# Kernel tuning notes

Measured on AMD Instinct MI355X. Metric: run time of the kernel, lower is better.

The kernel has to match this reference:

```python
import jax, jax.numpy as jnp
import numpy as np

QLEN, MLEN = 1024, 1024
KLEN = QLEN + MLEN
BSZ = 2
D_MODEL = 1024
N_HEAD, D_HEAD = 16, 64


def setup_inputs() -> dict:
    key = jax.random.key(0)
    ks = jax.random.split(key, 8)
    s = 0.02
    return {
        "w": jax.random.normal(ks[0], (KLEN, BSZ, D_MODEL), jnp.float32),
        "r": jax.random.normal(ks[1], (KLEN, D_MODEL), jnp.float32),
        "r_w_bias": jax.random.normal(ks[2], (N_HEAD, D_HEAD), jnp.float32) * s,
        "r_r_bias": jax.random.normal(ks[3], (N_HEAD, D_HEAD), jnp.float32) * s,
        "Wq": jax.random.normal(ks[4], (D_MODEL, N_HEAD * D_HEAD), jnp.float32) * s,
        "Wkv": jax.random.normal(ks[5], (D_MODEL, 2 * N_HEAD * D_HEAD), jnp.float32) * s,
        "Wr": jax.random.normal(ks[6], (D_MODEL, N_HEAD * D_HEAD), jnp.float32) * s,
        "Wo": jax.random.normal(ks[7], (N_HEAD * D_HEAD, D_MODEL), jnp.float32) * s,
        "qlen": QLEN,
    }


def _rel_shift(x):
    # x: [qlen, klen, bsz, n_head]. Pad one zero column at the front of the
    # key axis, reinterpret flat layout as [klen+1, qlen, ...], drop row 0.
    q, k, b, n = x.shape
    x_pad = jnp.pad(x, ((0, 0), (1, 0), (0, 0), (0, 0)))
    return x_pad.reshape(k + 1, q, b, n)[1:].reshape(q, k, b, n)


def reference(w, r, r_w_bias, r_r_bias, Wq, Wkv, Wr, Wo, qlen):
    klen, bsz, _ = w.shape
    rlen = r.shape[0]
    scale = 1.0 / (D_HEAD ** 0.5)

    w_head_q = (w[-qlen:] @ Wq).reshape(qlen, bsz, N_HEAD, D_HEAD)
    kv = w @ Wkv
    w_head_k = kv[..., : N_HEAD * D_HEAD].reshape(klen, bsz, N_HEAD, D_HEAD)
    w_head_v = kv[..., N_HEAD * D_HEAD :].reshape(klen, bsz, N_HEAD, D_HEAD)
    r_head_k = (r @ Wr).reshape(rlen, N_HEAD, D_HEAD)

    AC = jnp.einsum("ibnd,jbnd->ijbn", w_head_q + r_w_bias, w_head_k)
    BD = jnp.einsum("ibnd,jnd->ijbn", w_head_q + r_r_bias, r_head_k)
    attn_score = (AC + _rel_shift(BD)) * scale

    attn_prob = jax.nn.softmax(attn_score, axis=1)
    attn_vec = jnp.einsum("ijbn,jbnd->ibnd", attn_prob, w_head_v)
    attn_vec = attn_vec.reshape(qlen, bsz, N_HEAD * D_HEAD)
    return attn_vec @ Wo
```

## Files before the change

### kernel.cpp

```cpp
#include <hip/hip_runtime.h>
#include <hip/hip_bf16.h>


#define QLENC 1024
#define KLENC 2048
#define BSZC 2
#define DMODELC 1024
#define NHC 16
#define DHC 64

typedef _Float16 half_t;
typedef __attribute__((ext_vector_type(8))) _Float16 f16x8;
typedef __attribute__((ext_vector_type(4))) float f32x4;

__device__ __forceinline__ void async_copy16(const half_t* g, half_t* l) {
    __builtin_amdgcn_global_load_lds(
        (const __attribute__((address_space(1))) void*)g,
        (__attribute__((address_space(3))) void*)l,
        16, 0, 0);
}

__global__ __launch_bounds__(256) void prep(
    const float* __restrict__ w, const float* __restrict__ r,
    const float* __restrict__ Wq, const float* __restrict__ Wkv,
    const float* __restrict__ Wr, const float* __restrict__ Wo,
    half_t* __restrict__ wh, half_t* __restrict__ rh,
    half_t* __restrict__ WqT, half_t* __restrict__ WkvT,
    half_t* __restrict__ WrT, half_t* __restrict__ WoT) {
    __shared__ __attribute__((aligned(16))) half_t T[64][72];
    int bx = blockIdx.x, t = threadIdx.x;
    if (bx < 3072) {
        const float* s; half_t* d; size_t base;
        if (bx < 2048) { s = w; d = wh; base = (size_t)bx * 2048; }
        else           { s = r; d = rh; base = (size_t)(bx - 2048) * 2048; }
        size_t i = base + (size_t)t * 8;
        const float4* sp = (const float4*)(s + i);
        float4 f0 = sp[0], f1 = sp[1];
        half_t h[8];
        h[0] = (half_t)f0.x; h[1] = (half_t)f0.y; h[2] = (half_t)f0.z; h[3] = (half_t)f0.w;
        h[4] = (half_t)f1.x; h[5] = (half_t)f1.y; h[6] = (half_t)f1.z; h[7] = (half_t)f1.w;
        *(uint4*)(d + i) = *(uint4*)&h[0];
        return;
    }
    int b2 = bx - 3072;
    const float* W; half_t* Wt; int N, tx, ty;
    if (b2 < 256)       { W = Wq;  Wt = WqT;  N = 1024; tx = b2 & 15;         ty = b2 >> 4; }
    else if (b2 < 768)  { int c = b2 - 256;  W = Wkv; Wt = WkvT; N = 2048; tx = c & 31; ty = c >> 5; }
    else if (b2 < 1024) { int c = b2 - 768;  W = Wr;  Wt = WrT;  N = 1024; tx = c & 15; ty = c >> 4; }
    else                { int c = b2 - 1024; W = Wo;  Wt = WoT;  N = 1024; tx = c & 15; ty = c >> 4; }
    const int K = 1024;
    int n0 = tx * 64, k0 = ty * 64;
    int r_ = t >> 2, c_ = (t & 3) << 4;
    const float4* s = (const float4*)&W[(size_t)(k0 + r_) * N + n0 + c_];
    float4 f0 = s[0], f1 = s[1], f2 = s[2], f3 = s[3];
    half_t h[16];
    h[0] = (half_t)f0.x; h[1] = (half_t)f0.y; h[2] = (half_t)f0.z; h[3] = (half_t)f0.w;
    h[4] = (half_t)f1.x; h[5] = (half_t)f1.y; h[6] = (half_t)f1.z; h[7] = (half_t)f1.w;
    h[8] = (half_t)f2.x; h[9] = (half_t)f2.y; h[10] = (half_t)f2.z; h[11] = (half_t)f2.w;
    h[12] = (half_t)f3.x; h[13] = (half_t)f3.y; h[14] = (half_t)f3.z; h[15] = (half_t)f3.w;
    *(uint4*)&T[r_][c_] = *(uint4*)&h[0];
    *(uint4*)&T[r_][c_ + 8] = *(uint4*)&h[8];
    __syncthreads();
    half_t vals[16];
#pragma unroll
    for (int u = 0; u < 16; u++) vals[u] = T[c_ + u][r_];
    *(uint4*)&Wt[(size_t)(n0 + r_) * K + k0 + c_] = *(uint4*)&vals[0];
    *(uint4*)&Wt[(size_t)(n0 + r_) * K + k0 + c_ + 8] = *(uint4*)&vals[8];
}

__global__ __launch_bounds__(256) void proj_fused(
    const half_t* __restrict__ wh, const half_t* __restrict__ rh,
    const half_t* __restrict__ WqT, const half_t* __restrict__ WkvT,
    const half_t* __restrict__ WrT,
    half_t* __restrict__ qw, half_t* __restrict__ qr,
    half_t* __restrict__ kh, half_t* __restrict__ vt,
    half_t* __restrict__ rk,
    const float* __restrict__ rwb, const float* __restrict__ rrb) {
    __shared__ __attribute__((aligned(16))) half_t SM[128 * 136];
    half_t (*As)[64] = (half_t(*)[64])SM;
    half_t (*Bs)[64] = (half_t(*)[64])(SM + 128 * 64);
    half_t (*LT)[136] = (half_t(*)[136])SM;

    int bid = blockIdx.x;
    int mode, tx, ty;
    const half_t* A; const half_t* Bt;
    if (bid < 512)      { mode = 1; tx = bid & 15, ty = bid >> 4; A = wh; Bt = WkvT; }
    else if (bid < 640) { int c = bid - 512; mode = 0; tx = c & 7; ty = c >> 3;
                          A = wh + (size_t)QLENC * BSZC * DMODELC; Bt = WqT; }
    else                { int c = bid - 640; mode = 2; tx = c & 7; ty = c >> 3;
                          A = rh; Bt = WrT; }

    int t = threadIdx.x;
    int w = t >> 6, ln = t & 63, quad = ln >> 4, l15 = ln & 15;
    int m0 = ty * 128, n0 = tx * 128;
    int rbase = 64 * (w >> 1), cbase = 64 * (w & 1);
    int lrow = ln >> 3, lcol = (ln & 7) * 8;

    f32x4 acc[4][4];
#pragma unroll
    for (int i = 0; i < 4; i++)
#pragma unroll
        for (int j = 0; j < 4; j++) acc[i][j] = (f32x4){0.f, 0.f, 0.f, 0.f};

    for (int k0 = 0; k0 < 1024; k0 += 64) {
        __syncthreads();
#pragma unroll
        for (int j = 0; j < 4; j++) {
            int r8 = w * 32 + j * 8;
            async_copy16(&A[(size_t)(m0 + r8 + lrow) * 1024 + k0 + lcol], &As[r8][0]);
            async_copy16(&Bt[(size_t)(n0 + r8 + lrow) * 1024 + k0 + lcol], &Bs[r8][0]);
        }
        __syncthreads();
#pragma unroll
        for (int kk = 0; kk < 2; kk++) {
            f16x8 af[4], bfr[4];
#pragma unroll
            for (int rb = 0; rb < 4; rb++)
                af[rb] = *(const f16x8*)&As[rbase + rb * 16 + l15][kk * 32 + quad * 8];
#pragma unroll
            for (int cb = 0; cb < 4; cb++)
                bfr[cb] = *(const f16x8*)&Bs[cbase + cb * 16 + l15][kk * 32 + quad * 8];
#pragma unroll
            for (int rb = 0; rb < 4; rb++)
#pragma unroll
                for (int cb = 0; cb < 4; cb++)
                    acc[rb][cb] = __builtin_amdgcn_mfma_f32_16x16x32_f16(
                        af[rb], bfr[cb], acc[rb][cb], 0, 0, 0);
        }
    }

    if (mode == 1 && tx >= 8) {
        __syncthreads();
#pragma unroll
        for (int rb = 0; rb < 4; rb++)
#pragma unroll
            for (int cb = 0; cb < 4; cb++)
#pragma unroll
                for (int reg = 0; reg < 4; reg++) {
                    int lr_ = rbase + 16 * rb + quad * 4 + reg;
                    int lc_ = cbase + 16 * cb + l15;
                    LT[lc_][lr_] = (half_t)acc[rb][cb][reg];
                }
        __syncthreads();
#pragma unroll
        for (int pass = 0; pass < 8; pass++) {
            int g = pass * 32 + (t >> 3), s_ = t & 7;
            int lc_ = g >> 1, b_ = g & 1;
            half_t tmp[8];
#pragma unroll
            for (int k = 0; k < 8; k++) tmp[k] = LT[lc_][b_ + 2 * (s_ * 8 + k)];
            int gc = n0 - 1024 + lc_;
            int hh = gc >> 6, d_ = gc & 63;
            int p0 = (m0 >> 1) + s_ * 8;
            *(uint4*)&vt[(((size_t)(b_ * NHC + hh)) * DHC + d_) * KLENC + p0] = *(uint4*)&tmp[0];
        }
        return;
    }

#pragma unroll
    for (int rb = 0; rb < 4; rb++)
#pragma unroll
        for (int cb = 0; cb < 4; cb++)
#pragma unroll
            for (int reg = 0; reg < 4; reg++) {
                int gr = m0 + rbase + 16 * rb + quad * 4 + reg;
                int gc = n0 + cbase + 16 * cb + l15;
                float v = acc[rb][cb][reg];
                if (mode == 1) {
                    int p_ = gr >> 1, b_ = gr & 1;
                    int n_ = gc >> 6, d_ = gc & 63;
                    kh[(((size_t)(b_ * NHC + n_)) * KLENC + p_) * DHC + d_] = (half_t)v;
                } else if (mode == 0) {
                    int p_ = gr >> 1, b_ = gr & 1, n_ = gc >> 6, d_ = gc & 63;
                    size_t idx = (((size_t)(b_ * NHC + n_)) * QLENC + p_) * DHC + d_;
                    qw[idx] = (half_t)(v + rwb[gc]);
                    qr[idx] = (half_t)(v + rrb[gc]);
                } else {
                    int n_ = gc >> 6, d_ = gc & 63;
                    rk[(((size_t)n_) * KLENC + gr) * DHC + d_] = (half_t)v;
                }
            }
}

__global__ __launch_bounds__(256) void gemm_out(
    const half_t* __restrict__ A, const half_t* __restrict__ Bt,
    float* __restrict__ o) {
    __shared__ __attribute__((aligned(16))) half_t As[128][64];
    __shared__ __attribute__((aligned(16))) half_t Bs[128][64];

    int t = threadIdx.x;
    int w = t >> 6, ln = t & 63, quad = ln >> 4, l15 = ln & 15;
    int m0 = blockIdx.y * 128, n0 = blockIdx.x * 128;
    int rbase = 64 * (w >> 1), cbase = 64 * (w & 1);
    int lrow = ln >> 3, lcol = (ln & 7) * 8;

    f32x4 acc[4][4];
#pragma unroll
    for (int i = 0; i < 4; i++)
#pragma unroll
        for (int j = 0; j < 4; j++) acc[i][j] = (f32x4){0.f, 0.f, 0.f, 0.f};

    for (int k0 = 0; k0 < 1024; k0 += 64) {
        __syncthreads();
#pragma unroll
        for (int j = 0; j < 4; j++) {
            int r8 = w * 32 + j * 8;
            async_copy16(&A[(size_t)(m0 + r8 + lrow) * 1024 + k0 + lcol], &As[r8][0]);
            async_copy16(&Bt[(size_t)(n0 + r8 + lrow) * 1024 + k0 + lcol], &Bs[r8][0]);
        }
        __syncthreads();
#pragma unroll
        for (int kk = 0; kk < 2; kk++) {
            f16x8 af[4], bfr[4];
#pragma unroll
            for (int rb = 0; rb < 4; rb++)
                af[rb] = *(const f16x8*)&As[rbase + rb * 16 + l15][kk * 32 + quad * 8];
#pragma unroll
            for (int cb = 0; cb < 4; cb++)
                bfr[cb] = *(const f16x8*)&Bs[cbase + cb * 16 + l15][kk * 32 + quad * 8];
#pragma unroll
            for (int rb = 0; rb < 4; rb++)
#pragma unroll
                for (int cb = 0; cb < 4; cb++)
                    acc[rb][cb] = __builtin_amdgcn_mfma_f32_16x16x32_f16(
                        af[rb], bfr[cb], acc[rb][cb], 0, 0, 0);
        }
    }

#pragma unroll
    for (int rb = 0; rb < 4; rb++)
#pragma unroll
        for (int cb = 0; cb < 4; cb++)
#pragma unroll
            for (int reg = 0; reg < 4; reg++) {
                int gr = m0 + rbase + 16 * rb + quad * 4 + reg;
                int gc = n0 + cbase + 16 * cb + l15;
                o[(size_t)gr * 1024 + gc] = acc[rb][cb][reg];
            }
}

__global__ __launch_bounds__(256, 3) void attn_fused(
    const half_t* __restrict__ qw, const half_t* __restrict__ qr,
    const half_t* __restrict__ kh, const half_t* __restrict__ vt,
    const half_t* __restrict__ rk, half_t* __restrict__ av) {
    __shared__ __attribute__((aligned(16))) half_t Ks[64][72];
    __shared__ __attribute__((aligned(16))) half_t Vs[64][72];
    __shared__ __attribute__((aligned(16))) half_t RKs[128][72];
    __shared__ __attribute__((aligned(16))) half_t TP[4][16][88];

    int n = blockIdx.x, i0 = blockIdx.y * 64, b = blockIdx.z;
    int t = threadIdx.x, w = t >> 6, ln = t & 63, quad = ln >> 4, l15 = ln & 15;
    int lr = t >> 2, lc = (t & 3) << 4;
    int q4 = quad * 4;
    int wq = w * 16 + q4;
    size_t bn = (size_t)(b * NHC + n);
    const half_t* rkn = rk + (size_t)n * KLENC * DHC;
    half_t (*TPw)[88] = TP[w];

    f16x8 aqw[2], aq1[2], aq2[2];
    {
        int row1 = i0 + w * 16 + l15;
        int row2 = row1 + 1; if (row2 > QLENC - 1) row2 = QLENC - 1;
#pragma unroll
        for (int kk = 0; kk < 2; kk++) {
            aqw[kk] = *(const f16x8*)&qw[((bn * QLENC) + row1) * DHC + kk * 32 + quad * 8];
            aq1[kk] = *(const f16x8*)&qr[((bn * QLENC) + row1) * DHC + kk * 32 + quad * 8];
            aq2[kk] = *(const f16x8*)&qr[((bn * QLENC) + row2) * DHC + kk * 32 + quad * 8];
        }
    }

    int rrl = t >> 1, rh = (t & 1) * 32;

    uint4 pk0, pk1, pv0, pv1, pr0, pr1, pr2, pr3;
    {
        int D = 0 - i0;
        int mb = (D <= 1024) ? (960 + D) : (D - 1089);
        int rrow = mb + rrl; rrow = rrow < 0 ? 0 : (rrow > KLENC - 1 ? KLENC - 1 : rrow);
        const uint4* ks = (const uint4*)&kh[((bn * KLENC) + 0 + lr) * DHC + lc];
        const uint4* vs = (const uint4*)&vt[((bn * DHC) + lr) * KLENC + 0 + lc];
        pk0 = ks[0]; pk1 = ks[1]; pv0 = vs[0]; pv1 = vs[1];
        const uint4* rs = (const uint4*)&rkn[(size_t)rrow * DHC + rh];
        pr0 = rs[0]; pr1 = rs[1]; pr2 = rs[2]; pr3 = rs[3];
    }

    f32x4 O[4];
#pragma unroll
    for (int i = 0; i < 4; i++) O[i] = (f32x4){0.f, 0.f, 0.f, 0.f};
    float lsum[4] = {0.f, 0.f, 0.f, 0.f};
    const float scale = 0.125f;

    for (int jt = 0; jt < KLENC / 64; jt++) {
        int j0 = jt * 64;
        int D = j0 - i0;
        bool need1 = (D <= 1024), need2 = (D >= 1024);

        __syncthreads();
        *(uint4*)&Ks[lr][lc] = pk0; *(uint4*)&Ks[lr][lc + 8] = pk1;
        *(uint4*)&Vs[lr][lc] = pv0; *(uint4*)&Vs[lr][lc + 8] = pv1;
        *(uint4*)&RKs[rrl][rh] = pr0;      *(uint4*)&RKs[rrl][rh + 8] = pr1;
        *(uint4*)&RKs[rrl][rh + 16] = pr2; *(uint4*)&RKs[rrl][rh + 24] = pr3;
        __syncthreads();

        if (jt + 1 < KLENC / 64) {
            int j0n = j0 + 64, Dn = j0n - i0;
            int mbn = (Dn <= 1024) ? (960 + Dn) : (Dn - 1089);
            int rrown = mbn + rrl; rrown = rrown < 0 ? 0 : (rrown > KLENC - 1 ? KLENC - 1 : rrown);
            const uint4* ks = (const uint4*)&kh[((bn * KLENC) + j0n + lr) * DHC + lc];
            const uint4* vs = (const uint4*)&vt[((bn * DHC) + lr) * KLENC + j0n + lc];
            pk0 = ks[0]; pk1 = ks[1]; pv0 = vs[0]; pv1 = vs[1];
            const uint4* rs = (const uint4*)&rkn[(size_t)rrown * DHC + rh];
            pr0 = rs[0]; pr1 = rs[1]; pr2 = rs[2]; pr3 = rs[3];
        }

        f32x4 sa[4];
#pragma unroll
        for (int cb = 0; cb < 4; cb++) sa[cb] = (f32x4){0.f, 0.f, 0.f, 0.f};
#pragma unroll
        for (int kk = 0; kk < 2; kk++) {
#pragma unroll
            for (int cb = 0; cb < 4; cb++) {
                f16x8 bk = *(const f16x8*)&Ks[cb * 16 + l15][kk * 32 + quad * 8];
                sa[cb] = __builtin_amdgcn_mfma_f32_16x16x32_f16(aqw[kk], bk, sa[cb], 0, 0, 0);
            }
        }

        float bdv[4][4];
#pragma unroll
        for (int cb = 0; cb < 4; cb++)
#pragma unroll
            for (int reg = 0; reg < 4; reg++) bdv[cb][reg] = 0.f;

        if (need1) {
            f32x4 tacc[5];
#pragma unroll
            for (int c = 0; c < 5; c++) tacc[c] = (f32x4){0.f, 0.f, 0.f, 0.f};
#pragma unroll
            for (int kk = 0; kk < 2; kk++) {
#pragma unroll
                for (int c = 0; c < 5; c++) {
                    f16x8 bk = *(const f16x8*)&RKs[(3 - w + c) * 16 + l15][kk * 32 + quad * 8];
                    tacc[c] = __builtin_amdgcn_mfma_f32_16x16x32_f16(aq1[kk], bk, tacc[c], 0, 0, 0);
                }
            }
#pragma unroll
            for (int c = 0; c < 5; c++)
#pragma unroll
                for (int reg = 0; reg < 4; reg++)
                    TPw[q4 + reg][c * 16 + l15] = (half_t)tacc[c][reg];
#pragma unroll
            for (int reg = 0; reg < 4; reg++) {
                int icl = q4 + reg, ic = w * 16 + icl;
#pragma unroll
                for (int cb = 0; cb < 4; cb++) {
                    int jc = cb * 16 + l15;
                    int delta = D + jc - ic;
                    if (delta <= 1024) bdv[cb][reg] = (float)TPw[icl][15 + jc - icl];
                }
            }
        }
        if (need2) {
            if (need1) {
                int mb2 = D - 1089;
                int rrow2 = mb2 + rrl; rrow2 = rrow2 < 0 ? 0 : (rrow2 > KLENC - 1 ? KLENC - 1 : rrow2);
                const uint4* rs2 = (const uint4*)&rkn[(size_t)rrow2 * DHC + rh];
                uint4 t0 = rs2[0], t1 = rs2[1], t2 = rs2[2], t3 = rs2[3];
                __syncthreads();
                *(uint4*)&RKs[rrl][rh] = t0;      *(uint4*)&RKs[rrl][rh + 8] = t1;
                *(uint4*)&RKs[rrl][rh + 16] = t2; *(uint4*)&RKs[rrl][rh + 24] = t3;
                __syncthreads();
            }
            f32x4 tacc[5];
#pragma unroll
            for (int c = 0; c < 5; c++) tacc[c] = (f32x4){0.f, 0.f, 0.f, 0.f};
#pragma unroll
            for (int kk = 0; kk < 2; kk++) {
#pragma unroll
                for (int c = 0; c < 5; c++) {
                    f16x8 bk = *(const f16x8*)&RKs[(3 - w + c) * 16 + l15][kk * 32 + quad * 8];
                    tacc[c] = __builtin_amdgcn_mfma_f32_16x16x32_f16(aq2[kk], bk, tacc[c], 0, 0, 0);
                }
            }
#pragma unroll
            for (int c = 0; c < 5; c++)
#pragma unroll
                for (int reg = 0; reg < 4; reg++)
                    TPw[q4 + reg][c * 16 + l15] = (half_t)tacc[c][reg];
#pragma unroll
            for (int reg = 0; reg < 4; reg++) {
                int icl = q4 + reg, ic = w * 16 + icl;
#pragma unroll
                for (int cb = 0; cb < 4; cb++) {
                    int jc = cb * 16 + l15;
                    int delta = D + jc - ic;
                    if (delta >= 1026) bdv[cb][reg] = (float)TPw[icl][15 + jc - icl];
                }
            }
        }

        float p[4][4];
#pragma unroll
        for (int reg = 0; reg < 4; reg++) {
            float ps = 0.f;
#pragma unroll
            for (int cb = 0; cb < 4; cb++) {
                float e = __expf((sa[cb][reg] + bdv[cb][reg]) * scale);
                e = fminf(e, 60000.f);
                p[cb][reg] = e; ps += e;
            }
            lsum[reg] += ps;
        }

#pragma unroll
        for (int cb = 0; cb < 4; cb++)
#pragma unroll
            for (int reg = 0; reg < 4; reg++)
                TPw[q4 + reg][cb * 16 + l15] = (half_t)p[cb][reg];
#pragma unroll
        for (int kk = 0; kk < 2; kk++) {
            f16x8 pa = *(const f16x8*)&TPw[l15][kk * 32 + quad * 8];
#pragma unroll
            for (int db = 0; db < 4; db++) {
                f16x8 vb = *(const f16x8*)&Vs[db * 16 + l15][kk * 32 + quad * 8];
                O[db] = __builtin_amdgcn_mfma_f32_16x16x32_f16(pa, vb, O[db], 0, 0, 0);
            }
        }
    }

    float inv[4];
#pragma unroll
    for (int reg = 0; reg < 4; reg++) {
        float tot = lsum[reg];
#pragma unroll
        for (int off = 1; off < 16; off <<= 1) tot += __shfl_xor(tot, off, 64);
        inv[reg] = 1.0f / tot;
    }
#pragma unroll
    for (int db = 0; db < 4; db++)
#pragma unroll
        for (int reg = 0; reg < 4; reg++) {
            int i = i0 + wq + reg;
            int col = n * 64 + db * 16 + l15;
            av[((size_t)i * BSZC + b) * DMODELC + col] = (half_t)(O[db][reg] * inv[reg]);
        }
}

extern "C" void kernel_launch(void* const* d_in, const int* in_sizes, int n_in,
                              void* d_out, int out_size, void* d_ws, size_t ws_size,
                              hipStream_t stream) {
    const float* w   = (const float*)d_in[0];
    const float* r   = (const float*)d_in[1];
    const float* rwb = (const float*)d_in[2];
    const float* rrb = (const float*)d_in[3];
    const float* Wq  = (const float*)d_in[4];
    const float* Wkv = (const float*)d_in[5];
    const float* Wr  = (const float*)d_in[6];
    const float* Wo  = (const float*)d_in[7];
    float* out = (float*)d_out;

    half_t* ws = (half_t*)d_ws;
    half_t* qw   = ws; ws += (size_t)BSZC * NHC * QLENC * DHC;
    half_t* qr   = ws; ws += (size_t)BSZC * NHC * QLENC * DHC;
    half_t* kh   = ws; ws += (size_t)BSZC * NHC * KLENC * DHC;
    half_t* vt   = ws; ws += (size_t)BSZC * NHC * KLENC * DHC;
    half_t* rk   = ws; ws += (size_t)NHC * KLENC * DHC;
    half_t* av   = ws; ws += (size_t)QLENC * BSZC * DMODELC;
    half_t* WqT  = ws; ws += (size_t)DMODELC * DMODELC;
    half_t* WkvT = ws; ws += (size_t)2 * DMODELC * DMODELC;
    half_t* WrT  = ws; ws += (size_t)DMODELC * DMODELC;
    half_t* WoT  = ws; ws += (size_t)DMODELC * DMODELC;
    half_t* wh   = ws; ws += (size_t)KLENC * BSZC * DMODELC;
    half_t* rh   = ws; ws += (size_t)KLENC * DMODELC;

    dim3 blk(256);
    prep<<<dim3(4352), blk, 0, stream>>>(w, r, Wq, Wkv, Wr, Wo,
                                         wh, rh, WqT, WkvT, WrT, WoT);
    proj_fused<<<dim3(768), blk, 0, stream>>>(
        wh, rh, WqT, WkvT, WrT, qw, qr, kh, vt, rk, rwb, rrb);
    attn_fused<<<dim3(NHC, QLENC / 64, BSZC), blk, 0, stream>>>(
        qw, qr, kh, vt, rk, av);
    gemm_out<<<dim3(8, 16), blk, 0, stream>>>(av, WoT, out);

    (void)in_sizes; (void)n_in; (void)out_size; (void)ws_size;
}
```

Baseline: 270.6 us.

## Double-buffer K/V in LDS and load relative keys directly into registers

```diff
diff --git a/kernel.cpp b/kernel.cpp
--- a/kernel.cpp
+++ b/kernel.cpp
@@ -239,13 +239,12 @@
             }
 }
 
-__global__ __launch_bounds__(256, 3) void attn_fused(
+__global__ __launch_bounds__(256, 2) void attn_fused(
     const half_t* __restrict__ qw, const half_t* __restrict__ qr,
     const half_t* __restrict__ kh, const half_t* __restrict__ vt,
     const half_t* __restrict__ rk, half_t* __restrict__ av) {
-    __shared__ __attribute__((aligned(16))) half_t Ks[64][72];
-    __shared__ __attribute__((aligned(16))) half_t Vs[64][72];
-    __shared__ __attribute__((aligned(16))) half_t RKs[128][72];
+    __shared__ __attribute__((aligned(16))) half_t Ks[2][64][72];
+    __shared__ __attribute__((aligned(16))) half_t Vs[2][64][72];
     __shared__ __attribute__((aligned(16))) half_t TP[4][16][88];
 
     int n = blockIdx.x, i0 = blockIdx.y * 64, b = blockIdx.z;
@@ -269,18 +268,26 @@
         }
     }
 
-    int rrl = t >> 1, rh = (t & 1) * 32;
-
-    uint4 pk0, pk1, pv0, pv1, pr0, pr1, pr2, pr3;
+#define LOAD_RK(MB, DST)                                                      \
+    do {                                                                      \
+        _Pragma("unroll")                                                     \
+        for (int c_ = 0; c_ < 5; c_++) {                                      \
+            int rg = (MB) + (3 - w + c_) * 16 + l15;                          \
+            rg = rg < 0 ? 0 : (rg > KLENC - 1 ? KLENC - 1 : rg);              \
+            const half_t* rp = &rkn[(size_t)rg * DHC + quad * 8];             \
+            DST[c_ * 2]     = *(const f16x8*)rp;                              \
+            DST[c_ * 2 + 1] = *(const f16x8*)(rp + 32);                       \
+        }                                                                     \
+    } while (0)
+
+    uint4 pk0, pk1, pv0, pv1;
+    f16x8 rka[10], rkb[10];
     {
-        int D = 0 - i0;
-        int mb = (D <= 1024) ? (960 + D) : (D - 1089);
-        int rrow = mb + rrl; rrow = rrow < 0 ? 0 : (rrow > KLENC - 1 ? KLENC - 1 : rrow);
         const uint4* ks = (const uint4*)&kh[((bn * KLENC) + 0 + lr) * DHC + lc];
         const uint4* vs = (const uint4*)&vt[((bn * DHC) + lr) * KLENC + 0 + lc];
         pk0 = ks[0]; pk1 = ks[1]; pv0 = vs[0]; pv1 = vs[1];
-        const uint4* rs = (const uint4*)&rkn[(size_t)rrow * DHC + rh];
-        pr0 = rs[0]; pr1 = rs[1]; pr2 = rs[2]; pr3 = rs[3];
+        int D0 = 0 - i0;
+        LOAD_RK(960 + D0, rka);
     }
 
     f32x4 O[4];
@@ -289,142 +296,128 @@
     float lsum[4] = {0.f, 0.f, 0.f, 0.f};
     const float scale = 0.125f;
 
-    for (int jt = 0; jt < KLENC / 64; jt++) {
-        int j0 = jt * 64;
-        int D = j0 - i0;
-        bool need1 = (D <= 1024), need2 = (D >= 1024);
-
-        __syncthreads();
-        *(uint4*)&Ks[lr][lc] = pk0; *(uint4*)&Ks[lr][lc + 8] = pk1;
-        *(uint4*)&Vs[lr][lc] = pv0; *(uint4*)&Vs[lr][lc + 8] = pv1;
-        *(uint4*)&RKs[rrl][rh] = pr0;      *(uint4*)&RKs[rrl][rh + 8] = pr1;
-        *(uint4*)&RKs[rrl][rh + 16] = pr2; *(uint4*)&RKs[rrl][rh + 24] = pr3;
-        __syncthreads();
-
-        if (jt + 1 < KLENC / 64) {
-            int j0n = j0 + 64, Dn = j0n - i0;
-            int mbn = (Dn <= 1024) ? (960 + Dn) : (Dn - 1089);
-            int rrown = mbn + rrl; rrown = rrown < 0 ? 0 : (rrown > KLENC - 1 ? KLENC - 1 : rrown);
-            const uint4* ks = (const uint4*)&kh[((bn * KLENC) + j0n + lr) * DHC + lc];
-            const uint4* vs = (const uint4*)&vt[((bn * DHC) + lr) * KLENC + j0n + lc];
-            pk0 = ks[0]; pk1 = ks[1]; pv0 = vs[0]; pv1 = vs[1];
-            const uint4* rs = (const uint4*)&rkn[(size_t)rrown * DHC + rh];
-            pr0 = rs[0]; pr1 = rs[1]; pr2 = rs[2]; pr3 = rs[3];
-        }
-
-        f32x4 sa[4];
-#pragma unroll
-        for (int cb = 0; cb < 4; cb++) sa[cb] = (f32x4){0.f, 0.f, 0.f, 0.f};
-#pragma unroll
-        for (int kk = 0; kk < 2; kk++) {
-#pragma unroll
-            for (int cb = 0; cb < 4; cb++) {
-                f16x8 bk = *(const f16x8*)&Ks[cb * 16 + l15][kk * 32 + quad * 8];
-                sa[cb] = __builtin_amdgcn_mfma_f32_16x16x32_f16(aqw[kk], bk, sa[cb], 0, 0, 0);
-            }
-        }
-
-        float bdv[4][4];
-#pragma unroll
-        for (int cb = 0; cb < 4; cb++)
-#pragma unroll
-            for (int reg = 0; reg < 4; reg++) bdv[cb][reg] = 0.f;
-
-        if (need1) {
-            f32x4 tacc[5];
-#pragma unroll
-            for (int c = 0; c < 5; c++) tacc[c] = (f32x4){0.f, 0.f, 0.f, 0.f};
-#pragma unroll
-            for (int kk = 0; kk < 2; kk++) {
-#pragma unroll
-                for (int c = 0; c < 5; c++) {
-                    f16x8 bk = *(const f16x8*)&RKs[(3 - w + c) * 16 + l15][kk * 32 + quad * 8];
-                    tacc[c] = __builtin_amdgcn_mfma_f32_16x16x32_f16(aq1[kk], bk, tacc[c], 0, 0, 0);
-                }
-            }
-#pragma unroll
-            for (int c = 0; c < 5; c++)
-#pragma unroll
-                for (int reg = 0; reg < 4; reg++)
-                    TPw[q4 + reg][c * 16 + l15] = (half_t)tacc[c][reg];
-#pragma unroll
-            for (int reg = 0; reg < 4; reg++) {
-                int icl = q4 + reg, ic = w * 16 + icl;
-#pragma unroll
-                for (int cb = 0; cb < 4; cb++) {
-                    int jc = cb * 16 + l15;
-                    int delta = D + jc - ic;
-                    if (delta <= 1024) bdv[cb][reg] = (float)TPw[icl][15 + jc - icl];
-                }
-            }
-        }
-        if (need2) {
-            if (need1) {
-                int mb2 = D - 1089;
-                int rrow2 = mb2 + rrl; rrow2 = rrow2 < 0 ? 0 : (rrow2 > KLENC - 1 ? KLENC - 1 : rrow2);
-                const uint4* rs2 = (const uint4*)&rkn[(size_t)rrow2 * DHC + rh];
-                uint4 t0 = rs2[0], t1 = rs2[1], t2 = rs2[2], t3 = rs2[3];
-                __syncthreads();
-                *(uint4*)&RKs[rrl][rh] = t0;      *(uint4*)&RKs[rrl][rh + 8] = t1;
-                *(uint4*)&RKs[rrl][rh + 16] = t2; *(uint4*)&RKs[rrl][rh + 24] = t3;
-                __syncthreads();
-            }
-            f32x4 tacc[5];
-#pragma unroll
-            for (int c = 0; c < 5; c++) tacc[c] = (f32x4){0.f, 0.f, 0.f, 0.f};
-#pragma unroll
-            for (int kk = 0; kk < 2; kk++) {
-#pragma unroll
-                for (int c = 0; c < 5; c++) {
-                    f16x8 bk = *(const f16x8*)&RKs[(3 - w + c) * 16 + l15][kk * 32 + quad * 8];
-                    tacc[c] = __builtin_amdgcn_mfma_f32_16x16x32_f16(aq2[kk], bk, tacc[c], 0, 0, 0);
-                }
-            }
-#pragma unroll
-            for (int c = 0; c < 5; c++)
-#pragma unroll
-                for (int reg = 0; reg < 4; reg++)
-                    TPw[q4 + reg][c * 16 + l15] = (half_t)tacc[c][reg];
-#pragma unroll
-            for (int reg = 0; reg < 4; reg++) {
-                int icl = q4 + reg, ic = w * 16 + icl;
-#pragma unroll
-                for (int cb = 0; cb < 4; cb++) {
-                    int jc = cb * 16 + l15;
-                    int delta = D + jc - ic;
-                    if (delta >= 1026) bdv[cb][reg] = (float)TPw[icl][15 + jc - icl];
-                }
-            }
-        }
-
-        float p[4][4];
-#pragma unroll
-        for (int reg = 0; reg < 4; reg++) {
-            float ps = 0.f;
-#pragma unroll
-            for (int cb = 0; cb < 4; cb++) {
-                float e = __expf((sa[cb][reg] + bdv[cb][reg]) * scale);
-                e = fminf(e, 60000.f);
-                p[cb][reg] = e; ps += e;
-            }
-            lsum[reg] += ps;
-        }
-
-#pragma unroll
-        for (int cb = 0; cb < 4; cb++)
-#pragma unroll
-            for (int reg = 0; reg < 4; reg++)
-                TPw[q4 + reg][cb * 16 + l15] = (half_t)p[cb][reg];
-#pragma unroll
-        for (int kk = 0; kk < 2; kk++) {
-            f16x8 pa = *(const f16x8*)&TPw[l15][kk * 32 + quad * 8];
-#pragma unroll
-            for (int db = 0; db < 4; db++) {
-                f16x8 vb = *(const f16x8*)&Vs[db * 16 + l15][kk * 32 + quad * 8];
-                O[db] = __builtin_amdgcn_mfma_f32_16x16x32_f16(pa, vb, O[db], 0, 0, 0);
-            }
-        }
-    }
+#define TILE_BODY(JT, BUF, RKC, RKN)                                          \
+    do {                                                                      \
+        int j0 = (JT) * 64;                                                   \
+        int D = j0 - i0;                                                      \
+        bool need1 = (D <= 1024), need2 = (D >= 1024);     \
+        *(uint4*)&Ks[BUF][lr][lc] = pk0; *(uint4*)&Ks[BUF][lr][lc + 8] = pk1; \
+        *(uint4*)&Vs[BUF][lr][lc] = pv0; *(uint4*)&Vs[BUF][lr][lc + 8] = pv1; \
+        __syncthreads();                                                      \
+        if ((JT) + 1 < KLENC / 64) {                                          \
+            int j0n = j0 + 64, Dn = j0n - i0;                                 \
+            const uint4* ksp = (const uint4*)&kh[((bn * KLENC) + j0n + lr) * DHC + lc]; \
+            const uint4* vsp = (const uint4*)&vt[((bn * DHC) + lr) * KLENC + j0n + lc]; \
+            pk0 = ksp[0]; pk1 = ksp[1]; pv0 = vsp[0]; pv1 = vsp[1];           \
+            int mbn = (Dn <= 1024) ? (960 + Dn) : (Dn - 1089);                \
+            LOAD_RK(mbn, RKN);                                                \
+        }                                                                     \
+        f32x4 sa[4];                                                          \
+        _Pragma("unroll")                                                     \
+        for (int cb = 0; cb < 4; cb++) sa[cb] = (f32x4){0.f, 0.f, 0.f, 0.f};  \
+        _Pragma("unroll")                                                     \
+        for (int kk = 0; kk < 2; kk++) {                                      \
+            _Pragma("unroll")                                                 \
+            for (int cb = 0; cb < 4; cb++) {                                  \
+                f16x8 bk = *(const f16x8*)&Ks[BUF][cb * 16 + l15][kk * 32 + quad * 8]; \
+                sa[cb] = __builtin_amdgcn_mfma_f32_16x16x32_f16(aqw[kk], bk, sa[cb], 0, 0, 0); \
+            }                                                                 \
+        }                                                                     \
+        float bdv[4][4];                                                      \
+        _Pragma("unroll")                                                     \
+        for (int cb = 0; cb < 4; cb++)                                        \
+            _Pragma("unroll")                                                 \
+            for (int reg = 0; reg < 4; reg++) bdv[cb][reg] = 0.f;             \
+        {    \
+            f16x8 aqA0 = need1 ? aq1[0] : aq2[0];                             \
+            f16x8 aqA1 = need1 ? aq1[1] : aq2[1];                             \
+            f32x4 tacc[5];                                                    \
+            _Pragma("unroll")                                                 \
+            for (int c = 0; c < 5; c++) tacc[c] = (f32x4){0.f, 0.f, 0.f, 0.f}; \
+            _Pragma("unroll")                                                 \
+            for (int c = 0; c < 5; c++) {                                     \
+                tacc[c] = __builtin_amdgcn_mfma_f32_16x16x32_f16(aqA0, RKC[c * 2], tacc[c], 0, 0, 0); \
+                tacc[c] = __builtin_amdgcn_mfma_f32_16x16x32_f16(aqA1, RKC[c * 2 + 1], tacc[c], 0, 0, 0); \
+            }                                                                 \
+            _Pragma("unroll")                                                 \
+            for (int c = 0; c < 5; c++)                                       \
+                _Pragma("unroll")                                             \
+                for (int reg = 0; reg < 4; reg++)                             \
+                    TPw[q4 + reg][c * 16 + l15] = (half_t)tacc[c][reg];       \
+            _Pragma("unroll")                                                 \
+            for (int reg = 0; reg < 4; reg++) {                               \
+                int icl = q4 + reg, ic = w * 16 + icl;                        \
+                _Pragma("unroll")                                             \
+                for (int cb = 0; cb < 4; cb++) {                              \
+                    int jc = cb * 16 + l15;                                   \
+                    int delta = D + jc - ic;                                  \
+                    bool take = need1 ? (delta <= 1024) : (delta >= 1026);    \
+                    if (take) bdv[cb][reg] = (float)TPw[icl][15 + jc - icl];  \
+                }                                                             \
+            }                                                                 \
+        }                                                                     \
+        if (need1 && need2) {     \
+            f16x8 rkm[10];                                                    \
+            LOAD_RK(D - 1089, rkm);                                           \
+            f32x4 tacc[5];                                                    \
+            _Pragma("unroll")                                                 \
+            for (int c = 0; c < 5; c++) tacc[c] = (f32x4){0.f, 0.f, 0.f, 0.f}; \
+            _Pragma("unroll")                                                 \
+            for (int c = 0; c < 5; c++) {                                     \
+                tacc[c] = __builtin_amdgcn_mfma_f32_16x16x32_f16(aq2[0], rkm[c * 2], tacc[c], 0, 0, 0); \
+                tacc[c] = __builtin_amdgcn_mfma_f32_16x16x32_f16(aq2[1], rkm[c * 2 + 1], tacc[c], 0, 0, 0); \
+            }                                                                 \
+            _Pragma("unroll")                                                 \
+            for (int c = 0; c < 5; c++)                                       \
+                _Pragma("unroll")                                             \
+                for (int reg = 0; reg < 4; reg++)                             \
+                    TPw[q4 + reg][c * 16 + l15] = (half_t)tacc[c][reg];       \
+            _Pragma("unroll")                                                 \
+            for (int reg = 0; reg < 4; reg++) {                               \
+                int icl = q4 + reg, ic = w * 16 + icl;                        \
+                _Pragma("unroll")                                             \
+                for (int cb = 0; cb < 4; cb++) {                              \
+                    int jc = cb * 16 + l15;                                   \
+                    int delta = D + jc - ic;                                  \
+                    if (delta >= 1026) bdv[cb][reg] = (float)TPw[icl][15 + jc - icl]; \
+                }                                                             \
+            }                                                                 \
+        }                                                                     \
+        float p[4][4];                                                        \
+        _Pragma("unroll")                                                     \
+        for (int reg = 0; reg < 4; reg++) {                                   \
+            float ps = 0.f;                                                   \
+            _Pragma("unroll")                                                 \
+            for (int cb = 0; cb < 4; cb++) {                                  \
+                float e = __expf((sa[cb][reg] + bdv[cb][reg]) * scale);       \
+                e = fminf(e, 60000.f);                                        \
+                p[cb][reg] = e; ps += e;                                      \
+            }                                                                 \
+            lsum[reg] += ps;                                                  \
+        }                                                                     \
+        _Pragma("unroll")                                                     \
+        for (int cb = 0; cb < 4; cb++)                                        \
+            _Pragma("unroll")                                                 \
+            for (int reg = 0; reg < 4; reg++)                                 \
+                TPw[q4 + reg][cb * 16 + l15] = (half_t)p[cb][reg];            \
+        _Pragma("unroll")                                                     \
+        for (int kk = 0; kk < 2; kk++) {                                      \
+            f16x8 pa = *(const f16x8*)&TPw[l15][kk * 32 + quad * 8];          \
+            _Pragma("unroll")                                                 \
+            for (int db = 0; db < 4; db++) {                                  \
+                f16x8 vb = *(const f16x8*)&Vs[BUF][db * 16 + l15][kk * 32 + quad * 8]; \
+                O[db] = __builtin_amdgcn_mfma_f32_16x16x32_f16(pa, vb, O[db], 0, 0, 0); \
+            }                                                                 \
+        }                                                                     \
+    } while (0)
+
+#pragma unroll 1
+    for (int jt = 0; jt < KLENC / 64; jt += 2) {
+        TILE_BODY(jt, 0, rka, rkb);
+        TILE_BODY(jt + 1, 1, rkb, rka);
+    }
+#undef TILE_BODY
+#undef LOAD_RK
 
     float inv[4];
 #pragma unroll
```

New measurement: 284.0 us. +5.0%, slower.

## Double-buffer K/V/RK tiles with async global-to-LDS copies and XOR swizzle

Applied to the files above, without the earlier changes.

```diff
diff --git a/kernel.cpp b/kernel.cpp
--- a/kernel.cpp
+++ b/kernel.cpp
@@ -239,24 +239,52 @@
             }
 }
 
-__global__ __launch_bounds__(256, 3) void attn_fused(
+__global__ __launch_bounds__(256, 2) void attn_fused(
     const half_t* __restrict__ qw, const half_t* __restrict__ qr,
     const half_t* __restrict__ kh, const half_t* __restrict__ vt,
     const half_t* __restrict__ rk, half_t* __restrict__ av) {
-    __shared__ __attribute__((aligned(16))) half_t Ks[64][72];
-    __shared__ __attribute__((aligned(16))) half_t Vs[64][72];
-    __shared__ __attribute__((aligned(16))) half_t RKs[128][72];
+    __shared__ __attribute__((aligned(16))) half_t KsL[2][64 * 64];
+    __shared__ __attribute__((aligned(16))) half_t VsL[2][64 * 64];
+    __shared__ __attribute__((aligned(16))) half_t RKL[2][128 * 64];
     __shared__ __attribute__((aligned(16))) half_t TP[4][16][88];
 
     int n = blockIdx.x, i0 = blockIdx.y * 64, b = blockIdx.z;
     int t = threadIdx.x, w = t >> 6, ln = t & 63, quad = ln >> 4, l15 = ln & 15;
-    int lr = t >> 2, lc = (t & 3) << 4;
     int q4 = quad * 4;
     int wq = w * 16 + q4;
     size_t bn = (size_t)(b * NHC + n);
     const half_t* rkn = rk + (size_t)n * KLENC * DHC;
     half_t (*TPw)[88] = TP[w];
 
+    int srow = ln >> 3;
+    int schalf = ((((ln & 7) * 16) ^ (srow << 4)) >> 1);
+    int sx = (l15 & 7) << 3;
+
+    const half_t* kbase = &kh[(bn * KLENC + w * 8 + srow) * DHC + schalf];
+    const half_t* vbase = &vt[((bn * DHC) + w * 8 + srow) * KLENC + schalf];
+
+#define STAGE_KV(J0, BUF)                                                     \
+    do {                                                                      \
+        _Pragma("unroll")                                                     \
+        for (int i_ = 0; i_ < 2; i_++) {                                      \
+            async_copy16(kbase + ((J0) + i_ * 32) * DHC,                      \
+                         &KsL[BUF][i_ * 2048 + w * 512]);                     \
+            async_copy16(vbase + (size_t)i_ * 32 * KLENC + (J0),              \
+                         &VsL[BUF][i_ * 2048 + w * 512]);                     \
+        }                                                                     \
+    } while (0)
+
+#define STAGE_RK(MB, BUF)                                                     \
+    do {                                                                      \
+        _Pragma("unroll")                                                     \
+        for (int i_ = 0; i_ < 4; i_++) {                                      \
+            int rg = (MB) + i_ * 32 + w * 8 + srow;                           \
+            rg = rg < 0 ? 0 : (rg > KLENC - 1 ? KLENC - 1 : rg);              \
+            async_copy16(&rkn[(size_t)rg * DHC + schalf],                     \
+                         &RKL[BUF][i_ * 2048 + w * 512]);                     \
+        }                                                                     \
+    } while (0)
+
     f16x8 aqw[2], aq1[2], aq2[2];
     {
         int row1 = i0 + w * 16 + l15;
@@ -269,19 +297,9 @@
         }
     }
 
-    int rrl = t >> 1, rh = (t & 1) * 32;
-
-    uint4 pk0, pk1, pv0, pv1, pr0, pr1, pr2, pr3;
-    {
-        int D = 0 - i0;
-        int mb = (D <= 1024) ? (960 + D) : (D - 1089);
-        int rrow = mb + rrl; rrow = rrow < 0 ? 0 : (rrow > KLENC - 1 ? KLENC - 1 : rrow);
-        const uint4* ks = (const uint4*)&kh[((bn * KLENC) + 0 + lr) * DHC + lc];
-        const uint4* vs = (const uint4*)&vt[((bn * DHC) + lr) * KLENC + 0 + lc];
-        pk0 = ks[0]; pk1 = ks[1]; pv0 = vs[0]; pv1 = vs[1];
-        const uint4* rs = (const uint4*)&rkn[(size_t)rrow * DHC + rh];
-        pr0 = rs[0]; pr1 = rs[1]; pr2 = rs[2]; pr3 = rs[3];
-    }
+    STAGE_KV(0, 0);
+    STAGE_RK(960 + (0 - i0), 0);
+    __syncthreads();
 
     f32x4 O[4];
 #pragma unroll
@@ -289,28 +307,22 @@
     float lsum[4] = {0.f, 0.f, 0.f, 0.f};
     const float scale = 0.125f;
 
+#pragma unroll 1
     for (int jt = 0; jt < KLENC / 64; jt++) {
+        int cur = jt & 1;
         int j0 = jt * 64;
         int D = j0 - i0;
         bool need1 = (D <= 1024), need2 = (D >= 1024);
 
-        __syncthreads();
-        *(uint4*)&Ks[lr][lc] = pk0; *(uint4*)&Ks[lr][lc + 8] = pk1;
-        *(uint4*)&Vs[lr][lc] = pv0; *(uint4*)&Vs[lr][lc + 8] = pv1;
-        *(uint4*)&RKs[rrl][rh] = pr0;      *(uint4*)&RKs[rrl][rh + 8] = pr1;
-        *(uint4*)&RKs[rrl][rh + 16] = pr2; *(uint4*)&RKs[rrl][rh + 24] = pr3;
-        __syncthreads();
-
         if (jt + 1 < KLENC / 64) {
-            int j0n = j0 + 64, Dn = j0n - i0;
-            int mbn = (Dn <= 1024) ? (960 + Dn) : (Dn - 1089);
-            int rrown = mbn + rrl; rrown = rrown < 0 ? 0 : (rrown > KLENC - 1 ? KLENC - 1 : rrown);
-            const uint4* ks = (const uint4*)&kh[((bn * KLENC) + j0n + lr) * DHC + lc];
-            const uint4* vs = (const uint4*)&vt[((bn * DHC) + lr) * KLENC + j0n + lc];
-            pk0 = ks[0]; pk1 = ks[1]; pv0 = vs[0]; pv1 = vs[1];
-            const uint4* rs = (const uint4*)&rkn[(size_t)rrown * DHC + rh];
-            pr0 = rs[0]; pr1 = rs[1]; pr2 = rs[2]; pr3 = rs[3];
-        }
+            int Dn = D + 64;
+            STAGE_KV(j0 + 64, cur ^ 1);
+            STAGE_RK((Dn <= 1024) ? (960 + Dn) : (Dn - 1089), cur ^ 1);
+        }
+
+        const half_t* Kb = KsL[cur];
+        const half_t* Vb = VsL[cur];
+        const half_t* Rb = RKL[cur];
 
         f32x4 sa[4];
 #pragma unroll
@@ -319,7 +331,7 @@
         for (int kk = 0; kk < 2; kk++) {
 #pragma unroll
             for (int cb = 0; cb < 4; cb++) {
-                f16x8 bk = *(const f16x8*)&Ks[cb * 16 + l15][kk * 32 + quad * 8];
+                f16x8 bk = *(const f16x8*)&Kb[(cb * 16 + l15) * 64 + ((kk * 32 + quad * 8) ^ sx)];
                 sa[cb] = __builtin_amdgcn_mfma_f32_16x16x32_f16(aqw[kk], bk, sa[cb], 0, 0, 0);
             }
         }
@@ -330,17 +342,18 @@
 #pragma unroll
             for (int reg = 0; reg < 4; reg++) bdv[cb][reg] = 0.f;
 
-        if (need1) {
+        {
+            f16x8 aqA0 = need1 ? aq1[0] : aq2[0];
+            f16x8 aqA1 = need1 ? aq1[1] : aq2[1];
             f32x4 tacc[5];
 #pragma unroll
             for (int c = 0; c < 5; c++) tacc[c] = (f32x4){0.f, 0.f, 0.f, 0.f};
 #pragma unroll
-            for (int kk = 0; kk < 2; kk++) {
-#pragma unroll
-                for (int c = 0; c < 5; c++) {
-                    f16x8 bk = *(const f16x8*)&RKs[(3 - w + c) * 16 + l15][kk * 32 + quad * 8];
-                    tacc[c] = __builtin_amdgcn_mfma_f32_16x16x32_f16(aq1[kk], bk, tacc[c], 0, 0, 0);
-                }
+            for (int c = 0; c < 5; c++) {
+                f16x8 b0 = *(const f16x8*)&Rb[((3 - w + c) * 16 + l15) * 64 + ((0 + quad * 8) ^ sx)];
+                f16x8 b1 = *(const f16x8*)&Rb[((3 - w + c) * 16 + l15) * 64 + ((32 + quad * 8) ^ sx)];
+                tacc[c] = __builtin_amdgcn_mfma_f32_16x16x32_f16(aqA0, b0, tacc[c], 0, 0, 0);
+                tacc[c] = __builtin_amdgcn_mfma_f32_16x16x32_f16(aqA1, b1, tacc[c], 0, 0, 0);
             }
 #pragma unroll
             for (int c = 0; c < 5; c++)
@@ -354,31 +367,24 @@
                 for (int cb = 0; cb < 4; cb++) {
                     int jc = cb * 16 + l15;
                     int delta = D + jc - ic;
-                    if (delta <= 1024) bdv[cb][reg] = (float)TPw[icl][15 + jc - icl];
+                    bool take = need1 ? (delta <= 1024) : (delta >= 1026);
+                    if (take) bdv[cb][reg] = (float)TPw[icl][15 + jc - icl];
                 }
             }
         }
-        if (need2) {
-            if (need1) {
-                int mb2 = D - 1089;
-                int rrow2 = mb2 + rrl; rrow2 = rrow2 < 0 ? 0 : (rrow2 > KLENC - 1 ? KLENC - 1 : rrow2);
-                const uint4* rs2 = (const uint4*)&rkn[(size_t)rrow2 * DHC + rh];
-                uint4 t0 = rs2[0], t1 = rs2[1], t2 = rs2[2], t3 = rs2[3];
-                __syncthreads();
-                *(uint4*)&RKs[rrl][rh] = t0;      *(uint4*)&RKs[rrl][rh + 8] = t1;
-                *(uint4*)&RKs[rrl][rh + 16] = t2; *(uint4*)&RKs[rrl][rh + 24] = t3;
-                __syncthreads();
-            }
+        if (need1 && need2) {
+            __syncthreads();
+            STAGE_RK(D - 1089, cur);
+            __syncthreads();
             f32x4 tacc[5];
 #pragma unroll
             for (int c = 0; c < 5; c++) tacc[c] = (f32x4){0.f, 0.f, 0.f, 0.f};
 #pragma unroll
-            for (int kk = 0; kk < 2; kk++) {
-#pragma unroll
-                for (int c = 0; c < 5; c++) {
-                    f16x8 bk = *(const f16x8*)&RKs[(3 - w + c) * 16 + l15][kk * 32 + quad * 8];
-                    tacc[c] = __builtin_amdgcn_mfma_f32_16x16x32_f16(aq2[kk], bk, tacc[c], 0, 0, 0);
-                }
+            for (int c = 0; c < 5; c++) {
+                f16x8 b0 = *(const f16x8*)&Rb[((3 - w + c) * 16 + l15) * 64 + ((0 + quad * 8) ^ sx)];
+                f16x8 b1 = *(const f16x8*)&Rb[((3 - w + c) * 16 + l15) * 64 + ((32 + quad * 8) ^ sx)];
+                tacc[c] = __builtin_amdgcn_mfma_f32_16x16x32_f16(aq2[0], b0, tacc[c], 0, 0, 0);
+                tacc[c] = __builtin_amdgcn_mfma_f32_16x16x32_f16(aq2[1], b1, tacc[c], 0, 0, 0);
             }
 #pragma unroll
             for (int c = 0; c < 5; c++)
@@ -420,11 +426,15 @@
             f16x8 pa = *(const f16x8*)&TPw[l15][kk * 32 + quad * 8];
 #pragma unroll
             for (int db = 0; db < 4; db++) {
-                f16x8 vb = *(const f16x8*)&Vs[db * 16 + l15][kk * 32 + quad * 8];
+                f16x8 vb = *(const f16x8*)&Vb[(db * 16 + l15) * 64 + ((kk * 32 + quad * 8) ^ sx)];
                 O[db] = __builtin_amdgcn_mfma_f32_16x16x32_f16(pa, vb, O[db], 0, 0, 0);
             }
         }
-    }
+
+        __syncthreads();
+    }
+#undef STAGE_KV
+#undef STAGE_RK
 
     float inv[4];
 #pragma unroll
```

After: 271.0 us. Within noise of the previous version (+0.2%).

## Split attention key range across two blocks and combine partial outputs

Applied to the files above, without the earlier changes.

```diff
diff --git a/kernel.cpp b/kernel.cpp
--- a/kernel.cpp
+++ b/kernel.cpp
@@ -242,13 +242,16 @@
 __global__ __launch_bounds__(256, 3) void attn_fused(
     const half_t* __restrict__ qw, const half_t* __restrict__ qr,
     const half_t* __restrict__ kh, const half_t* __restrict__ vt,
-    const half_t* __restrict__ rk, half_t* __restrict__ av) {
+    const half_t* __restrict__ rk, float* __restrict__ po,
+    float* __restrict__ pl) {
     __shared__ __attribute__((aligned(16))) half_t Ks[64][72];
     __shared__ __attribute__((aligned(16))) half_t Vs[64][72];
     __shared__ __attribute__((aligned(16))) half_t RKs[128][72];
     __shared__ __attribute__((aligned(16))) half_t TP[4][16][88];
 
-    int n = blockIdx.x, i0 = blockIdx.y * 64, b = blockIdx.z;
+    int n = blockIdx.x, i0 = blockIdx.y * 64;
+    int z = blockIdx.z, b = z >> 1, s = z & 1;
+    int jt0 = s * 16, jt1 = jt0 + 16;
     int t = threadIdx.x, w = t >> 6, ln = t & 63, quad = ln >> 4, l15 = ln & 15;
     int lr = t >> 2, lc = (t & 3) << 4;
     int q4 = quad * 4;
@@ -273,11 +276,12 @@
 
     uint4 pk0, pk1, pv0, pv1, pr0, pr1, pr2, pr3;
     {
-        int D = 0 - i0;
+        int j0 = jt0 * 64;
+        int D = j0 - i0;
         int mb = (D <= 1024) ? (960 + D) : (D - 1089);
         int rrow = mb + rrl; rrow = rrow < 0 ? 0 : (rrow > KLENC - 1 ? KLENC - 1 : rrow);
-        const uint4* ks = (const uint4*)&kh[((bn * KLENC) + 0 + lr) * DHC + lc];
-        const uint4* vs = (const uint4*)&vt[((bn * DHC) + lr) * KLENC + 0 + lc];
+        const uint4* ks = (const uint4*)&kh[((bn * KLENC) + j0 + lr) * DHC + lc];
+        const uint4* vs = (const uint4*)&vt[((bn * DHC) + lr) * KLENC + j0 + lc];
         pk0 = ks[0]; pk1 = ks[1]; pv0 = vs[0]; pv1 = vs[1];
         const uint4* rs = (const uint4*)&rkn[(size_t)rrow * DHC + rh];
         pr0 = rs[0]; pr1 = rs[1]; pr2 = rs[2]; pr3 = rs[3];
@@ -289,7 +293,7 @@
     float lsum[4] = {0.f, 0.f, 0.f, 0.f};
     const float scale = 0.125f;
 
-    for (int jt = 0; jt < KLENC / 64; jt++) {
+    for (int jt = jt0; jt < jt1; jt++) {
         int j0 = jt * 64;
         int D = j0 - i0;
         bool need1 = (D <= 1024), need2 = (D >= 1024);
@@ -301,7 +305,7 @@
         *(uint4*)&RKs[rrl][rh + 16] = pr2; *(uint4*)&RKs[rrl][rh + 24] = pr3;
         __syncthreads();
 
-        if (jt + 1 < KLENC / 64) {
+        if (jt + 1 < jt1) {
             int j0n = j0 + 64, Dn = j0n - i0;
             int mbn = (Dn <= 1024) ? (960 + Dn) : (Dn - 1089);
             int rrown = mbn + rrl; rrown = rrown < 0 ? 0 : (rrown > KLENC - 1 ? KLENC - 1 : rrown);
@@ -426,22 +430,43 @@
         }
     }
 
-    float inv[4];
+    size_t pobase = ((size_t)s * 32 + bn) * QLENC;
+#pragma unroll
+    for (int db = 0; db < 4; db++)
+#pragma unroll
+        for (int reg = 0; reg < 4; reg++)
+            po[(pobase + i0 + wq + reg) * 64 + db * 16 + l15] = O[db][reg];
 #pragma unroll
     for (int reg = 0; reg < 4; reg++) {
         float tot = lsum[reg];
 #pragma unroll
         for (int off = 1; off < 16; off <<= 1) tot += __shfl_xor(tot, off, 64);
-        inv[reg] = 1.0f / tot;
-    }
-#pragma unroll
-    for (int db = 0; db < 4; db++)
-#pragma unroll
-        for (int reg = 0; reg < 4; reg++) {
-            int i = i0 + wq + reg;
-            int col = n * 64 + db * 16 + l15;
-            av[((size_t)i * BSZC + b) * DMODELC + col] = (half_t)(O[db][reg] * inv[reg]);
-        }
+        if (l15 == 0) pl[pobase + i0 + wq + reg] = tot;
+    }
+}
+
+__global__ __launch_bounds__(256) void combine(
+    const float* __restrict__ po, const float* __restrict__ pl,
+    half_t* __restrict__ av) {
+    int gid = blockIdx.x * 256 + threadIdx.x;
+    int d0 = (gid & 7) * 8;
+    int i = (gid >> 3) & 1023;
+    int bn = gid >> 13;
+    size_t rowoff = (size_t)bn * QLENC + i;
+    size_t base = rowoff * 64 + d0;
+    const size_t S = (size_t)32 * QLENC * 64;
+    float4 a0 = *(const float4*)&po[base];
+    float4 a1 = *(const float4*)&po[base + 4];
+    float4 b0 = *(const float4*)&po[S + base];
+    float4 b1 = *(const float4*)&po[S + base + 4];
+    float invl = 1.0f / (pl[rowoff] + pl[(size_t)32 * QLENC + rowoff]);
+    half_t h[8];
+    h[0] = (half_t)((a0.x + b0.x) * invl); h[1] = (half_t)((a0.y + b0.y) * invl);
+    h[2] = (half_t)((a0.z + b0.z) * invl); h[3] = (half_t)((a0.w + b0.w) * invl);
+    h[4] = (half_t)((a1.x + b1.x) * invl); h[5] = (half_t)((a1.y + b1.y) * invl);
+    h[6] = (half_t)((a1.z + b1.z) * invl); h[7] = (half_t)((a1.w + b1.w) * invl);
+    int b = bn >> 4, n = bn & 15;
+    *(uint4*)&av[((size_t)i * BSZC + b) * DMODELC + n * 64 + d0] = *(uint4*)&h[0];
 }
 
 extern "C" void kernel_launch(void* const* d_in, const int* in_sizes, int n_in,
@@ -464,20 +489,24 @@
     half_t* vt   = ws; ws += (size_t)BSZC * NHC * KLENC * DHC;
     half_t* rk   = ws; ws += (size_t)NHC * KLENC * DHC;
     half_t* av   = ws; ws += (size_t)QLENC * BSZC * DMODELC;
+    half_t* WoT  = ws; ws += (size_t)DMODELC * DMODELC;
     half_t* WqT  = ws; ws += (size_t)DMODELC * DMODELC;
     half_t* WkvT = ws; ws += (size_t)2 * DMODELC * DMODELC;
     half_t* WrT  = ws; ws += (size_t)DMODELC * DMODELC;
-    half_t* WoT  = ws; ws += (size_t)DMODELC * DMODELC;
     half_t* wh   = ws; ws += (size_t)KLENC * BSZC * DMODELC;
     half_t* rh   = ws; ws += (size_t)KLENC * DMODELC;
+
+    float* po = (float*)WqT;
+    float* pl = po + (size_t)2 * 32 * QLENC * 64;
 
     dim3 blk(256);
     prep<<<dim3(4352), blk, 0, stream>>>(w, r, Wq, Wkv, Wr, Wo,
                                          wh, rh, WqT, WkvT, WrT, WoT);
     proj_fused<<<dim3(768), blk, 0, stream>>>(
         wh, rh, WqT, WkvT, WrT, qw, qr, kh, vt, rk, rwb, rrb);
-    attn_fused<<<dim3(NHC, QLENC / 64, BSZC), blk, 0, stream>>>(
-        qw, qr, kh, vt, rk, av);
+    attn_fused<<<dim3(NHC, QLENC / 64, BSZC * 2), blk, 0, stream>>>(
+        qw, qr, kh, vt, rk, po, pl);
+    combine<<<dim3(1024), blk, 0, stream>>>(po, pl, av);
     gemm_out<<<dim3(8, 16), blk, 0, stream>>>(av, WoT, out);
 
     (void)in_sizes; (void)n_in; (void)out_size; (void)ws_size;
```

Result: no change. 268.9 us (-0.6%).
